# Optimization experiments

Hardware: AMD Instinct MI355X
Metric: run time of the kernel (lower is better)

Reference implementation:

```python
import jax, jax.numpy as jnp
import numpy as np

N_NODES = 16384
HIDDEN = 512
INPUT = 512
MAX_CHILDREN = 4


def _build_tree(n, k, seed=0):
    """Random forest where every child index < parent index (topological order)."""
    rng = np.random.default_rng(seed)
    parent = np.minimum(np.arange(n - 1) + 1 + rng.integers(1, 16, size=n - 1), n - 1)
    child_idx = np.zeros((n, k), dtype=np.int32)
    cnt = np.zeros(n, dtype=np.int32)
    for j in range(n - 1):
        p = int(parent[j])
        if cnt[p] < k:
            child_idx[p, cnt[p]] = j
            cnt[p] += 1
    child_mask = (np.arange(k)[None, :] < cnt[:, None]).astype(np.int32)
    return child_idx, child_mask


def setup_inputs() -> dict:
    key = jax.random.key(0)
    ks = jax.random.split(key, 8)
    s_in = 1.0 / np.sqrt(INPUT)
    s_h = 1.0 / np.sqrt(HIDDEN)
    child_idx, child_mask = _build_tree(N_NODES, MAX_CHILDREN)
    return {
        "inputs": jax.random.normal(ks[0], (N_NODES, INPUT), jnp.float32),
        "i2h_weight": jax.random.uniform(ks[1], (4 * HIDDEN, INPUT), jnp.float32, -s_in, s_in),
        "i2h_bias": jax.random.uniform(ks[2], (4 * HIDDEN,), jnp.float32, -s_in, s_in),
        "hs2h_weight": jax.random.uniform(ks[3], (3 * HIDDEN, HIDDEN), jnp.float32, -s_h, s_h),
        "hs2h_bias": jax.random.uniform(ks[4], (3 * HIDDEN,), jnp.float32, -s_h, s_h),
        "hc2h_weight": jax.random.uniform(ks[5], (HIDDEN, HIDDEN), jnp.float32, -s_h, s_h),
        "hc2h_bias": jax.random.uniform(ks[6], (HIDDEN,), jnp.float32, -s_h, s_h),
        "child_idx": jnp.asarray(child_idx),
        "child_mask": jnp.asarray(child_mask),
    }


def reference(inputs, i2h_weight, i2h_bias, hs2h_weight, hs2h_bias,
              hc2h_weight, hc2h_bias, child_idx, child_mask):
    n, _ = inputs.shape
    hid = hc2h_weight.shape[0]
    # Batched input projection for all nodes at once: [N, 4H]
    i2h = inputs @ i2h_weight.T + i2h_bias
    i2h_i, i2h_f, i2h_u, i2h_o = jnp.split(i2h, 4, axis=1)
    i2h_iuo = jnp.concatenate([i2h_i, i2h_u, i2h_o], axis=1)  # [N, 3H]
    cmask = child_mask.astype(inputs.dtype)                    # [N, K]

    def step(carry, xs):
        H, C = carry
        idx, iuo_pre, f_pre, cidx, m = xs
        hc = H[cidx]                                  # [K, H] gathered child h
        cc = C[cidx]                                  # [K, H] gathered child c
        mm = m[:, None]
        hs = jnp.sum(hc * mm, axis=0)                 # child-sum h: [H]
        # per-child forget gate: sigmoid(W_x x + b_f + h_k @ W_hc)
        f = jax.nn.sigmoid(f_pre + hc2h_bias + hc @ hc2h_weight)  # [K, H]
        fc = jnp.sum(f * cc * mm, axis=0)             # [H]
        iuo = iuo_pre + hs @ hs2h_weight.T + hs2h_bias  # [3H]
        i_g, u_g, o_g = jnp.split(iuo, 3)
        next_c = jax.nn.sigmoid(i_g) * jnp.tanh(u_g) + fc
        next_h = jax.nn.sigmoid(o_g) * jnp.tanh(next_c)
        return (H.at[idx].set(next_h), C.at[idx].set(next_c)), None

    H0 = jnp.zeros((n, hid), inputs.dtype)
    C0 = jnp.zeros((n, hid), inputs.dtype)
    (H, C), _ = jax.lax.scan(step, (H0, C0),
                             (jnp.arange(n), i2h_iuo, i2h_f, child_idx, cmask))
    return jnp.stack([H, C])  # [2, N, H]: next_h and next_c for every node
```

## Files before the change

kernel.cpp:

```cpp
#include <hip/hip_runtime.h>
#include <math.h>
#include <stdint.h>

#define N_NODES 16384
#define HID 512
#define G4 2048
#define MAXC 4

#define T_TEAMS 16
#define S_WGS 16
#define NWG 256
#define BLK 512
#define NSUB 16
#define ECH 32

#define SENT 0xFFFFFFFFu

#define AT_LDF(p)   __hip_atomic_load((p), __ATOMIC_RELAXED, __HIP_MEMORY_SCOPE_AGENT)
#define AT_LDU(p)   __hip_atomic_load((p), __ATOMIC_RELAXED, __HIP_MEMORY_SCOPE_AGENT)
#define AT_STF(p,v) __hip_atomic_store((p), (v), __ATOMIC_RELAXED, __HIP_MEMORY_SCOPE_AGENT)

__device__ __forceinline__ float sigm(float x) { return 1.0f / (1.0f + __expf(-x)); }

#define BK 16
__global__ void __launch_bounds__(256) gemm_i2h(
    const float* __restrict__ A, const float* __restrict__ B,
    const float* __restrict__ bias, float* __restrict__ C)
{
  __shared__ float As[BK][68];
  __shared__ float Bs[BK][68];
  const int tid = threadIdx.x;
  const int tx = tid & 15, ty = tid >> 4;
  const int rowBase = blockIdx.y * 64, colBase = blockIdx.x * 64;
  const int r = tid >> 2;
  const int kk = (tid & 3) << 2;
  float acc[4][4] = {};

  for (int k0 = 0; k0 < 512; k0 += BK) {
    float4 a4 = *(const float4*)&A[(size_t)(rowBase + r) * 512 + k0 + kk];
    float4 b4 = *(const float4*)&B[(size_t)(colBase + r) * 512 + k0 + kk];
    __syncthreads();
    As[kk + 0][r] = a4.x; As[kk + 1][r] = a4.y; As[kk + 2][r] = a4.z; As[kk + 3][r] = a4.w;
    Bs[kk + 0][r] = b4.x; Bs[kk + 1][r] = b4.y; Bs[kk + 2][r] = b4.z; Bs[kk + 3][r] = b4.w;
    __syncthreads();
#pragma unroll
    for (int k = 0; k < BK; k++) {
      float4 av = *(const float4*)&As[k][ty << 2];
      float4 bv = *(const float4*)&Bs[k][tx << 2];
      float a0 = av.x, a1 = av.y, a2 = av.z, a3 = av.w;
      float b0 = bv.x, b1 = bv.y, b2 = bv.z, b3 = bv.w;
      acc[0][0] += a0 * b0; acc[0][1] += a0 * b1; acc[0][2] += a0 * b2; acc[0][3] += a0 * b3;
      acc[1][0] += a1 * b0; acc[1][1] += a1 * b1; acc[1][2] += a1 * b2; acc[1][3] += a1 * b3;
      acc[2][0] += a2 * b0; acc[2][1] += a2 * b1; acc[2][2] += a2 * b2; acc[2][3] += a2 * b3;
      acc[3][0] += a3 * b0; acc[3][1] += a3 * b1; acc[3][2] += a3 * b2; acc[3][3] += a3 * b3;
    }
  }
#pragma unroll
  for (int i = 0; i < 4; i++) {
    const int row = rowBase + (ty << 2) + i;
    const int col = colBase + (tx << 2);
    float4 o;
    o.x = acc[i][0] + bias[col + 0];
    o.y = acc[i][1] + bias[col + 1];
    o.z = acc[i][2] + bias[col + 2];
    o.w = acc[i][3] + bias[col + 3];
    *(float4*)&C[(size_t)row * G4 + col] = o;
  }
}

template<int NC>
__device__ __forceinline__ void gates_lds(
    const float (*hch)[HID], int e0,
    const float4* wi, const float4* wu, const float4* wo, const float* wf,
    float& aI, float& aU, float& aO, float (&aF)[4])
{
#pragma unroll
  for (int q = 0; q < 8; q++) {
    float4 c0 = *(const float4*)&hch[0][e0 + 4 * q];
    float4 c1 = {0,0,0,0}, c2 = {0,0,0,0}, c3 = {0,0,0,0};
    if constexpr (NC > 1) c1 = *(const float4*)&hch[1][e0 + 4 * q];
    if constexpr (NC > 2) c2 = *(const float4*)&hch[2][e0 + 4 * q];
    if constexpr (NC > 3) c3 = *(const float4*)&hch[3][e0 + 4 * q];
    float sx = c0.x, sy = c0.y, sz = c0.z, sw = c0.w;
    if constexpr (NC > 1) { sx += c1.x; sy += c1.y; sz += c1.z; sw += c1.w; }
    if constexpr (NC > 2) { sx += c2.x; sy += c2.y; sz += c2.z; sw += c2.w; }
    if constexpr (NC > 3) { sx += c3.x; sy += c3.y; sz += c3.z; sw += c3.w; }
    aI += wi[q].x * sx; aI += wi[q].y * sy; aI += wi[q].z * sz; aI += wi[q].w * sw;
    aU += wu[q].x * sx; aU += wu[q].y * sy; aU += wu[q].z * sz; aU += wu[q].w * sw;
    aO += wo[q].x * sx; aO += wo[q].y * sy; aO += wo[q].z * sz; aO += wo[q].w * sw;
    aF[0] += wf[4*q+0] * c0.x; aF[0] += wf[4*q+1] * c0.y;
    aF[0] += wf[4*q+2] * c0.z; aF[0] += wf[4*q+3] * c0.w;
    if constexpr (NC > 1) {
      aF[1] += wf[4*q+0] * c1.x; aF[1] += wf[4*q+1] * c1.y;
      aF[1] += wf[4*q+2] * c1.z; aF[1] += wf[4*q+3] * c1.w;
    }
    if constexpr (NC > 2) {
      aF[2] += wf[4*q+0] * c2.x; aF[2] += wf[4*q+1] * c2.y;
      aF[2] += wf[4*q+2] * c2.z; aF[2] += wf[4*q+3] * c2.w;
    }
    if constexpr (NC > 3) {
      aF[3] += wf[4*q+0] * c3.x; aF[3] += wf[4*q+1] * c3.y;
      aF[3] += wf[4*q+2] * c3.z; aF[3] += wf[4*q+3] * c3.w;
    }
  }
}

__global__ void __launch_bounds__(BLK, 2) recur(
    const float* __restrict__ i2h,
    const float* __restrict__ hs2h_w, const float* __restrict__ hc2h_w,
    const float* __restrict__ hs2h_b, const float* __restrict__ hc2h_b,
    const int* __restrict__ child_idx, const int* __restrict__ child_mask,
    float* Hout, float* Cout)
{
  __shared__ float hch[MAXC][HID];
  __shared__ float chc[MAXC][32];
  __shared__ float4 redA[NSUB][32];
  __shared__ float4 redB[NSUB][32];

  const int tid = threadIdx.x;
  const int wg = blockIdx.x;
  const int team = wg & (T_TEAMS - 1);
  const int slice = wg >> 4;
  const int rr = tid & 31;
  const int sub = tid >> 5;
  const int rp = slice * 32 + rr;
  const int e0 = sub * ECH;
  const int lr = tid - slice * 32;

  float4 wi[8], wu[8], wo[8];
  float wf[32];
#pragma unroll
  for (int q = 0; q < 8; q++) {
    wi[q] = *(const float4*)&hs2h_w[(size_t)rp * HID + e0 + 4 * q];
    wu[q] = *(const float4*)&hs2h_w[(size_t)(512 + rp) * HID + e0 + 4 * q];
    wo[q] = *(const float4*)&hs2h_w[(size_t)(1024 + rp) * HID + e0 + 4 * q];
  }
#pragma unroll
  for (int e = 0; e < 32; e++)
    wf[e] = hc2h_w[(size_t)(e0 + e) * HID + rp];

  const int rpp = slice * 32 + tid;
  float bI = 0.f, bU = 0.f, bO = 0.f, bF = 0.f;
  if (tid < 32) {
    bI = hs2h_b[rpp]; bU = hs2h_b[512 + rpp];
    bO = hs2h_b[1024 + rpp]; bF = hc2h_b[rpp];
  }

  for (int j = team; j < N_NODES; j += T_TEAMS) {
    const int4 ci = *(const int4*)&child_idx[j * 4];
    const int4 cm = *(const int4*)&child_mask[j * 4];
    const int nc = cm.x + cm.y + cm.z + cm.w;
    const int cix[4] = {ci.x, ci.y, ci.z, ci.w};

    float ipre = 0.f, fpre = 0.f, upre = 0.f, opre = 0.f;
    if (tid < 32) {
      const size_t jb = (size_t)j * G4;
      ipre = i2h[jb + rpp];
      fpre = i2h[jb + 512 + rpp];
      upre = i2h[jb + 1024 + rpp];
      opre = i2h[jb + 1536 + rpp];
    }

    float aI = 0.f, aU = 0.f, aO = 0.f, aF[4] = {0.f, 0.f, 0.f, 0.f};

    if (nc > 0) {
#pragma unroll
      for (int k = 0; k < MAXC; k++) {
        if (k < nc) {
          const uint32_t* hp = (const uint32_t*)(Hout + (size_t)cix[k] * HID + tid);
          uint32_t v = AT_LDU(hp);
          while (v == SENT) { __builtin_amdgcn_s_sleep(1); v = AT_LDU(hp); }
          hch[k][tid] = __uint_as_float(v);
          if ((unsigned)lr < 32u)
            chc[k][lr] = AT_LDF(Cout + (size_t)cix[k] * HID + tid);
        }
      }
      __syncthreads();

      float cC0 = 0.f, cC1 = 0.f, cC2 = 0.f, cC3 = 0.f;
      if (tid < 32) {
        cC0 = chc[0][tid];
        if (nc > 1) cC1 = chc[1][tid];
        if (nc > 2) cC2 = chc[2][tid];
        if (nc > 3) cC3 = chc[3][tid];
      }

      switch (nc) {
        case 1: gates_lds<1>(hch, e0, wi, wu, wo, wf, aI, aU, aO, aF); break;
        case 2: gates_lds<2>(hch, e0, wi, wu, wo, wf, aI, aU, aO, aF); break;
        case 3: gates_lds<3>(hch, e0, wi, wu, wo, wf, aI, aU, aO, aF); break;
        default: gates_lds<4>(hch, e0, wi, wu, wo, wf, aI, aU, aO, aF); break;
      }
      redA[sub][rr] = make_float4(aI, aU, aO, aF[0]);
      redB[sub][rr] = make_float4(aF[1], aF[2], aF[3], 0.f);
      __syncthreads();

      if (tid < 32) {
        float sI = 0.f, sU = 0.f, sO = 0.f;
        float sF0 = 0.f, sF1 = 0.f, sF2 = 0.f, sF3 = 0.f;
#pragma unroll
        for (int s = 0; s < NSUB; s++) {
          float4 a = redA[s][tid];
          float4 b = redB[s][tid];
          sI += a.x; sU += a.y; sO += a.z; sF0 += a.w;
          sF1 += b.x; sF2 += b.y; sF3 += b.z;
        }
        const float ig = ipre + bI + sI;
        const float ug = upre + bU + sU;
        const float og = opre + bO + sO;
        float c = sigm(ig) * tanhf(ug);
        c += sigm(fpre + bF + sF0) * cC0;
        if (nc > 1) c += sigm(fpre + bF + sF1) * cC1;
        if (nc > 2) c += sigm(fpre + bF + sF2) * cC2;
        if (nc > 3) c += sigm(fpre + bF + sF3) * cC3;
        const float h = sigm(og) * tanhf(c);
        AT_STF(Cout + (size_t)j * HID + rpp, c);
        asm volatile("" ::: "memory");
        __builtin_amdgcn_s_waitcnt(0);
        asm volatile("" ::: "memory");
        AT_STF(Hout + (size_t)j * HID + rpp, h);
      }
    } else {
      if (tid < 32) {
        const float ig = ipre + bI;
        const float ug = upre + bU;
        const float og = opre + bO;
        const float c = sigm(ig) * tanhf(ug);
        const float h = sigm(og) * tanhf(c);
        AT_STF(Cout + (size_t)j * HID + rpp, c);
        asm volatile("" ::: "memory");
        __builtin_amdgcn_s_waitcnt(0);
        asm volatile("" ::: "memory");
        AT_STF(Hout + (size_t)j * HID + rpp, h);
      }
    }
  }
}

extern "C" void kernel_launch(void* const* d_in, const int* in_sizes, int n_in,
                              void* d_out, int out_size, void* d_ws, size_t ws_size,
                              hipStream_t stream) {
  const float* inputs    = (const float*)d_in[0];
  const float* i2h_w     = (const float*)d_in[1];
  const float* i2h_b     = (const float*)d_in[2];
  const float* hs2h_w    = (const float*)d_in[3];
  const float* hs2h_b    = (const float*)d_in[4];
  const float* hc2h_w    = (const float*)d_in[5];
  const float* hc2h_b    = (const float*)d_in[6];
  const int*   child_idx = (const int*)d_in[7];
  const int*   child_mask= (const int*)d_in[8];

  float* Hout = (float*)d_out;
  float* Cout = Hout + (size_t)N_NODES * HID;

  float* i2h = (float*)d_ws;

  hipMemsetAsync(Hout, 0xFF, (size_t)N_NODES * HID * sizeof(float), stream);

  dim3 ggrid(G4 / 64, N_NODES / 64);
  gemm_i2h<<<ggrid, 256, 0, stream>>>(inputs, i2h_w, i2h_b, i2h);
  recur<<<NWG, BLK, 0, stream>>>(i2h, hs2h_w, hc2h_w, hs2h_b, hc2h_b,
                                 child_idx, child_mask, Hout, Cout);
}
```

Baseline: 9.352 ms.

## Poll child H and C sentinels concurrently and drop store ordering waits

Result: faster. 8.993 ms (-3.8%).

```diff
diff --git a/kernel.cpp b/kernel.cpp
--- a/kernel.cpp
+++ b/kernel.cpp
@@ -16,7 +16,6 @@
 
 #define SENT 0xFFFFFFFFu
 
-#define AT_LDF(p)   __hip_atomic_load((p), __ATOMIC_RELAXED, __HIP_MEMORY_SCOPE_AGENT)
 #define AT_LDU(p)   __hip_atomic_load((p), __ATOMIC_RELAXED, __HIP_MEMORY_SCOPE_AGENT)
 #define AT_STF(p,v) __hip_atomic_store((p), (v), __ATOMIC_RELAXED, __HIP_MEMORY_SCOPE_AGENT)
 
@@ -105,6 +104,46 @@
   }
 }
 
+template<int NC>
+__device__ __forceinline__ void poll_stage(
+    const int* cix, int tid, int lr,
+    float (*hch)[HID], float (*chc)[32],
+    const float* Hout, const float* Cout)
+{
+  const uint32_t* hp[NC];
+  const uint32_t* cp[NC];
+#pragma unroll
+  for (int k = 0; k < NC; k++) {
+    hp[k] = (const uint32_t*)(Hout + (size_t)cix[k] * HID + tid);
+    cp[k] = (const uint32_t*)(Cout + (size_t)cix[k] * HID + tid);
+  }
+  unsigned hm = (1u << NC) - 1;
+  unsigned cm = ((unsigned)lr < 32u) ? (1u << NC) - 1 : 0u;
+  for (;;) {
+    uint32_t th[NC], tc[NC];
+#pragma unroll
+    for (int k = 0; k < NC; k++)
+      if (hm & (1u << k)) th[k] = AT_LDU(hp[k]);
+#pragma unroll
+    for (int k = 0; k < NC; k++)
+      if (cm & (1u << k)) tc[k] = AT_LDU(cp[k]);
+#pragma unroll
+    for (int k = 0; k < NC; k++)
+      if ((hm & (1u << k)) && th[k] != SENT) {
+        hch[k][tid] = __uint_as_float(th[k]);
+        hm &= ~(1u << k);
+      }
+#pragma unroll
+    for (int k = 0; k < NC; k++)
+      if ((cm & (1u << k)) && tc[k] != SENT) {
+        chc[k][lr] = __uint_as_float(tc[k]);
+        cm &= ~(1u << k);
+      }
+    if (!(hm | cm)) break;
+    __builtin_amdgcn_s_sleep(1);
+  }
+}
+
 __global__ void __launch_bounds__(BLK, 2) recur(
     const float* __restrict__ i2h,
     const float* __restrict__ hs2h_w, const float* __restrict__ hc2h_w,
@@ -164,16 +203,11 @@
     float aI = 0.f, aU = 0.f, aO = 0.f, aF[4] = {0.f, 0.f, 0.f, 0.f};
 
     if (nc > 0) {
-#pragma unroll
-      for (int k = 0; k < MAXC; k++) {
-        if (k < nc) {
-          const uint32_t* hp = (const uint32_t*)(Hout + (size_t)cix[k] * HID + tid);
-          uint32_t v = AT_LDU(hp);
-          while (v == SENT) { __builtin_amdgcn_s_sleep(1); v = AT_LDU(hp); }
-          hch[k][tid] = __uint_as_float(v);
-          if ((unsigned)lr < 32u)
-            chc[k][lr] = AT_LDF(Cout + (size_t)cix[k] * HID + tid);
-        }
+      switch (nc) {
+        case 1: poll_stage<1>(cix, tid, lr, hch, chc, Hout, Cout); break;
+        case 2: poll_stage<2>(cix, tid, lr, hch, chc, Hout, Cout); break;
+        case 3: poll_stage<3>(cix, tid, lr, hch, chc, Hout, Cout); break;
+        default: poll_stage<4>(cix, tid, lr, hch, chc, Hout, Cout); break;
       }
       __syncthreads();
 
@@ -215,22 +249,13 @@
         if (nc > 3) c += sigm(fpre + bF + sF3) * cC3;
         const float h = sigm(og) * tanhf(c);
         AT_STF(Cout + (size_t)j * HID + rpp, c);
-        asm volatile("" ::: "memory");
-        __builtin_amdgcn_s_waitcnt(0);
-        asm volatile("" ::: "memory");
         AT_STF(Hout + (size_t)j * HID + rpp, h);
       }
     } else {
       if (tid < 32) {
-        const float ig = ipre + bI;
-        const float ug = upre + bU;
-        const float og = opre + bO;
-        const float c = sigm(ig) * tanhf(ug);
-        const float h = sigm(og) * tanhf(c);
+        const float c = sigm(ipre + bI) * tanhf(upre + bU);
+        const float h = sigm(opre + bO) * tanhf(c);
         AT_STF(Cout + (size_t)j * HID + rpp, c);
-        asm volatile("" ::: "memory");
-        __builtin_amdgcn_s_waitcnt(0);
-        asm volatile("" ::: "memory");
         AT_STF(Hout + (size_t)j * HID + rpp, h);
       }
     }
@@ -255,7 +280,7 @@
 
   float* i2h = (float*)d_ws;
 
-  hipMemsetAsync(Hout, 0xFF, (size_t)N_NODES * HID * sizeof(float), stream);
+  hipMemsetAsync(d_out, 0xFF, (size_t)2 * N_NODES * HID * sizeof(float), stream);
 
   dim3 ggrid(G4 / 64, N_NODES / 64);
   gemm_i2h<<<ggrid, 256, 0, stream>>>(inputs, i2h_w, i2h_b, i2h);
```

## Replace per-element sentinel polling with per-node completion counters

Applied to the files above, without the earlier changes.

Measured after the change: 9.231 ms. No clear change (-1.3%).

```diff
diff --git a/kernel.cpp b/kernel.cpp
--- a/kernel.cpp
+++ b/kernel.cpp
@@ -14,10 +14,8 @@
 #define NSUB 16
 #define ECH 32
 
-#define SENT 0xFFFFFFFFu
-
+#define AT_LD(p)    __hip_atomic_load((p), __ATOMIC_RELAXED, __HIP_MEMORY_SCOPE_AGENT)
 #define AT_LDF(p)   __hip_atomic_load((p), __ATOMIC_RELAXED, __HIP_MEMORY_SCOPE_AGENT)
-#define AT_LDU(p)   __hip_atomic_load((p), __ATOMIC_RELAXED, __HIP_MEMORY_SCOPE_AGENT)
 #define AT_STF(p,v) __hip_atomic_store((p), (v), __ATOMIC_RELAXED, __HIP_MEMORY_SCOPE_AGENT)
 
 __device__ __forceinline__ float sigm(float x) { return 1.0f / (1.0f + __expf(-x)); }
@@ -110,10 +108,9 @@
     const float* __restrict__ hs2h_w, const float* __restrict__ hc2h_w,
     const float* __restrict__ hs2h_b, const float* __restrict__ hc2h_b,
     const int* __restrict__ child_idx, const int* __restrict__ child_mask,
-    float* Hout, float* Cout)
+    float* Hout, float* Cout, int* done)
 {
   __shared__ float hch[MAXC][HID];
-  __shared__ float chc[MAXC][32];
   __shared__ float4 redA[NSUB][32];
   __shared__ float4 redB[NSUB][32];
 
@@ -125,7 +122,6 @@
   const int sub = tid >> 5;
   const int rp = slice * 32 + rr;
   const int e0 = sub * ECH;
-  const int lr = tid - slice * 32;
 
   float4 wi[8], wu[8], wo[8];
   float wf[32];
@@ -162,28 +158,36 @@
     }
 
     float aI = 0.f, aU = 0.f, aO = 0.f, aF[4] = {0.f, 0.f, 0.f, 0.f};
+    float cC0 = 0.f, cC1 = 0.f, cC2 = 0.f, cC3 = 0.f;
 
     if (nc > 0) {
-#pragma unroll
-      for (int k = 0; k < MAXC; k++) {
-        if (k < nc) {
-          const uint32_t* hp = (const uint32_t*)(Hout + (size_t)cix[k] * HID + tid);
-          uint32_t v = AT_LDU(hp);
-          while (v == SENT) { __builtin_amdgcn_s_sleep(1); v = AT_LDU(hp); }
-          hch[k][tid] = __uint_as_float(v);
-          if ((unsigned)lr < 32u)
-            chc[k][lr] = AT_LDF(Cout + (size_t)cix[k] * HID + tid);
-        }
+      if (tid == BLK - 1) {
+        unsigned pend = (1u << nc) - 1;
+        do {
+          int v0 = 0, v1 = 0, v2 = 0, v3 = 0;
+          if (pend & 1u) v0 = AT_LD(done + cix[0]);
+          if (pend & 2u) v1 = AT_LD(done + cix[1]);
+          if (pend & 4u) v2 = AT_LD(done + cix[2]);
+          if (pend & 8u) v3 = AT_LD(done + cix[3]);
+          if ((pend & 1u) && v0 == S_WGS) pend &= ~1u;
+          if ((pend & 2u) && v1 == S_WGS) pend &= ~2u;
+          if ((pend & 4u) && v2 == S_WGS) pend &= ~4u;
+          if ((pend & 8u) && v3 == S_WGS) pend &= ~8u;
+          if (pend) __builtin_amdgcn_s_sleep(2);
+        } while (pend);
       }
       __syncthreads();
 
-      float cC0 = 0.f, cC1 = 0.f, cC2 = 0.f, cC3 = 0.f;
+#pragma unroll
+      for (int k = 0; k < MAXC; k++)
+        if (k < nc) hch[k][tid] = AT_LDF(Hout + (size_t)cix[k] * HID + tid);
       if (tid < 32) {
-        cC0 = chc[0][tid];
-        if (nc > 1) cC1 = chc[1][tid];
-        if (nc > 2) cC2 = chc[2][tid];
-        if (nc > 3) cC3 = chc[3][tid];
-      }
+        cC0 = AT_LDF(Cout + (size_t)cix[0] * HID + rpp);
+        if (nc > 1) cC1 = AT_LDF(Cout + (size_t)cix[1] * HID + rpp);
+        if (nc > 2) cC2 = AT_LDF(Cout + (size_t)cix[2] * HID + rpp);
+        if (nc > 3) cC3 = AT_LDF(Cout + (size_t)cix[3] * HID + rpp);
+      }
+      __syncthreads();
 
       switch (nc) {
         case 1: gates_lds<1>(hch, e0, wi, wu, wo, wf, aI, aU, aO, aF); break;
@@ -194,10 +198,12 @@
       redA[sub][rr] = make_float4(aI, aU, aO, aF[0]);
       redB[sub][rr] = make_float4(aF[1], aF[2], aF[3], 0.f);
       __syncthreads();
-
-      if (tid < 32) {
-        float sI = 0.f, sU = 0.f, sO = 0.f;
-        float sF0 = 0.f, sF1 = 0.f, sF2 = 0.f, sF3 = 0.f;
+    }
+
+    if (tid < 32) {
+      float sI = 0.f, sU = 0.f, sO = 0.f;
+      float sF0 = 0.f, sF1 = 0.f, sF2 = 0.f, sF3 = 0.f;
+      if (nc > 0) {
 #pragma unroll
         for (int s = 0; s < NSUB; s++) {
           float4 a = redA[s][tid];
@@ -205,34 +211,25 @@
           sI += a.x; sU += a.y; sO += a.z; sF0 += a.w;
           sF1 += b.x; sF2 += b.y; sF3 += b.z;
         }
-        const float ig = ipre + bI + sI;
-        const float ug = upre + bU + sU;
-        const float og = opre + bO + sO;
-        float c = sigm(ig) * tanhf(ug);
-        c += sigm(fpre + bF + sF0) * cC0;
-        if (nc > 1) c += sigm(fpre + bF + sF1) * cC1;
-        if (nc > 2) c += sigm(fpre + bF + sF2) * cC2;
-        if (nc > 3) c += sigm(fpre + bF + sF3) * cC3;
-        const float h = sigm(og) * tanhf(c);
-        AT_STF(Cout + (size_t)j * HID + rpp, c);
-        asm volatile("" ::: "memory");
-        __builtin_amdgcn_s_waitcnt(0);
-        asm volatile("" ::: "memory");
-        AT_STF(Hout + (size_t)j * HID + rpp, h);
-      }
-    } else {
-      if (tid < 32) {
-        const float ig = ipre + bI;
-        const float ug = upre + bU;
-        const float og = opre + bO;
-        const float c = sigm(ig) * tanhf(ug);
-        const float h = sigm(og) * tanhf(c);
-        AT_STF(Cout + (size_t)j * HID + rpp, c);
-        asm volatile("" ::: "memory");
-        __builtin_amdgcn_s_waitcnt(0);
-        asm volatile("" ::: "memory");
-        AT_STF(Hout + (size_t)j * HID + rpp, h);
-      }
+      }
+      const float ig = ipre + bI + sI;
+      const float ug = upre + bU + sU;
+      const float og = opre + bO + sO;
+      float c = sigm(ig) * tanhf(ug);
+      if (nc > 0) c += sigm(fpre + bF + sF0) * cC0;
+      if (nc > 1) c += sigm(fpre + bF + sF1) * cC1;
+      if (nc > 2) c += sigm(fpre + bF + sF2) * cC2;
+      if (nc > 3) c += sigm(fpre + bF + sF3) * cC3;
+      const float h = sigm(og) * tanhf(c);
+      AT_STF(Cout + (size_t)j * HID + rpp, c);
+      AT_STF(Hout + (size_t)j * HID + rpp, h);
+    }
+    if (tid < 32) {
+      asm volatile("" ::: "memory");
+      __builtin_amdgcn_s_waitcnt(0);
+      asm volatile("" ::: "memory");
+      if (tid == 0)
+        __hip_atomic_fetch_add(done + j, 1, __ATOMIC_RELAXED, __HIP_MEMORY_SCOPE_AGENT);
     }
   }
 }
@@ -253,12 +250,15 @@
   float* Hout = (float*)d_out;
   float* Cout = Hout + (size_t)N_NODES * HID;
 
-  float* i2h = (float*)d_ws;
-
-  hipMemsetAsync(Hout, 0xFF, (size_t)N_NODES * HID * sizeof(float), stream);
+  char* ws = (char*)d_ws;
+  const size_t i2h_bytes = (size_t)N_NODES * G4 * sizeof(float);
+  float* i2h = (float*)ws;
+  int*   done = (int*)(ws + i2h_bytes);
+
+  hipMemsetAsync(done, 0, N_NODES * sizeof(int), stream);
 
   dim3 ggrid(G4 / 64, N_NODES / 64);
   gemm_i2h<<<ggrid, 256, 0, stream>>>(inputs, i2h_w, i2h_b, i2h);
   recur<<<NWG, BLK, 0, stream>>>(i2h, hs2h_w, hc2h_w, hs2h_b, hc2h_b,
-                                 child_idx, child_mask, Hout, Cout);
-}
+                                 child_idx, child_mask, Hout, Cout, done);
+}
```
